# Optimization experiments

Measured on AMD Instinct MI355X. Metric: run time of the kernel, lower is better.

Reference implementation:

```python
import jax, jax.numpy as jnp
import numpy as np

CUTOFF = 1.5  # matches init cutoff
BIG = 1e6    # stand-in for masked-out (diagonal) distances


def _energy(positions, cell, sigma_matrix, epsilon_matrix, alpha_matrix, species):
    n = positions.shape[0]
    # pairwise displacements dr[i, j] = pos[j] - pos[i], minimum image under PBC
    dr = positions[None, :, :] - positions[:, None, :]          # [N, N, 3]
    inv_cell = jnp.linalg.inv(cell)
    frac = dr @ inv_cell
    frac = frac - jnp.round(frac)                               # minimum image
    dr = frac @ cell
    r2 = jnp.sum(dr * dr, axis=-1)                              # [N, N]
    eye = jnp.eye(n, dtype=bool)
    r = jnp.sqrt(jnp.where(eye, 1.0, r2))                       # safe sqrt on diag
    r = jnp.where(eye, BIG, r)                                  # mask self-pairs
    # species-pair parameter gather: [N, N]
    si, sj = species[:, None], species[None, :]
    sig = sigma_matrix[si, sj]
    eps = epsilon_matrix[si, sj]
    alp = alpha_matrix[si, sj]
    within = (r < CUTOFF) & (~eye)
    # soft-sphere pair energy: eps/alpha * (1 - r/sigma)^alpha for r < sigma
    f = jnp.maximum(1.0 - r / sig, 0.0)
    e = (eps / alp) * jnp.power(f, alp)
    e = jnp.where(within, e, 0.0)
    return jnp.sum(e) / 2.0


def setup_inputs() -> dict:
    key = jax.random.key(0)
    k1, k2, k3, k4, k5 = jax.random.split(key, 5)
    N, S = 4096, 8
    density = 0.8
    L = float((N / density) ** (1.0 / 3.0))
    positions = jax.random.uniform(k1, (N, 3), dtype=jnp.float32) * L
    cell = (L * jnp.eye(3)).astype(jnp.float32)
    species = jax.random.randint(k2, (N,), 0, S)

    def sym(k, base, scale):
        a = jax.random.uniform(k, (S, S), dtype=jnp.float32)
        a = 0.5 * (a + a.T)
        return base + scale * a

    sigma_matrix = sym(k3, 0.9, 0.2)    # ~1.0
    epsilon_matrix = sym(k4, 0.9, 0.2)  # ~1.0
    alpha_matrix = sym(k5, 2.0, 0.5)    # ~2.0-2.5
    return {
        "positions": positions,
        "cell": cell,
        "sigma_matrix": sigma_matrix,
        "epsilon_matrix": epsilon_matrix,
        "alpha_matrix": alpha_matrix,
        "species": species,
    }


def reference(positions, cell, sigma_matrix, epsilon_matrix, alpha_matrix, species):
    energy, g = jax.value_and_grad(
        lambda p: _energy(p, cell, sigma_matrix, epsilon_matrix, alpha_matrix, species)
    )(positions)
    forces = -g
    return energy, forces
```

## Files before the change

### kernel.cpp

```cpp
#include <hip/hip_runtime.h>


#define TI 256
#define TJ 64
#define CUT2 2.25f

__device__ __forceinline__ float fast_pow(float f, float e) {
    return __builtin_amdgcn_exp2f(e * __builtin_amdgcn_logf(f));
}

__global__ __launch_bounds__(TI) void soft_sphere_kernel(
    const float* __restrict__ pos,
    const float* __restrict__ cell,
    const float* __restrict__ sigm,
    const float* __restrict__ epsm,
    const float* __restrict__ alpm,
    const int*   __restrict__ spec,
    float*  __restrict__ out,
    float4* __restrict__ ws,
    int n)
{
    __shared__ float4 sh_pos[TJ];
    __shared__ float4 sh_tab[64];
    __shared__ float  sh_e[TI / 64];

    const int tid = threadIdx.x;
    const int j0  = blockIdx.y * TJ;

    if (tid < 64) {
        float sg = sigm[tid], ep = epsm[tid], al = alpm[tid];
        float inv_sg = 1.0f / sg;
        sh_tab[tid] = make_float4(inv_sg, al - 1.0f, ep / al, ep * inv_sg);
        int j = j0 + tid;
        sh_pos[tid] = make_float4(pos[3 * j + 0], pos[3 * j + 1],
                                  pos[3 * j + 2], __int_as_float(spec[j]));
    }

    const float m00 = cell[0], m01 = cell[1], m02 = cell[2];
    const float m10 = cell[3], m11 = cell[4], m12 = cell[5];
    const float m20 = cell[6], m21 = cell[7], m22 = cell[8];
    const bool diag = (m01 == 0.0f) & (m02 == 0.0f) & (m10 == 0.0f) &
                      (m12 == 0.0f) & (m20 == 0.0f) & (m21 == 0.0f);

    const int   i   = blockIdx.x * TI + tid;
    const float px  = pos[3 * i + 0];
    const float py  = pos[3 * i + 1];
    const float pz  = pos[3 * i + 2];
    const int   si8 = spec[i] << 3;

    __syncthreads();

    float e_acc = 0.0f, fxa = 0.0f, fya = 0.0f, fza = 0.0f;

    if (diag) {
        const float iLx = 1.0f / m00, iLy = 1.0f / m11, iLz = 1.0f / m22;
#pragma unroll 4
        for (int t = 0; t < TJ; ++t) {
            float4 pj = sh_pos[t];
            float dx = pj.x - px;
            float dy = pj.y - py;
            float dz = pj.z - pz;
            dx = fmaf(-rintf(dx * iLx), m00, dx);
            dy = fmaf(-rintf(dy * iLy), m11, dy);
            dz = fmaf(-rintf(dz * iLz), m22, dz);
            float r2 = fmaf(dx, dx, fmaf(dy, dy, dz * dz));
            if (r2 < CUT2 && (j0 + t) != i) {
                float4 tab = sh_tab[si8 + __float_as_int(pj.w)];
                float rinv = rsqrtf(r2);
                float r    = r2 * rinv;
                float f    = fmaf(-r, tab.x, 1.0f);
                if (f > 0.0f) {
                    float p = fast_pow(f, tab.y);
                    e_acc = fmaf(tab.z * p, f, e_acc);
                    float c = tab.w * p * rinv;
                    fxa = fmaf(-c, dx, fxa);
                    fya = fmaf(-c, dy, fya);
                    fza = fmaf(-c, dz, fza);
                }
            }
        }
    } else {
        const float det = m00 * (m11 * m22 - m12 * m21)
                        - m01 * (m10 * m22 - m12 * m20)
                        + m02 * (m10 * m21 - m11 * m20);
        const float rdet = 1.0f / det;
        const float i00 = (m11 * m22 - m12 * m21) * rdet;
        const float i01 = (m02 * m21 - m01 * m22) * rdet;
        const float i02 = (m01 * m12 - m02 * m11) * rdet;
        const float i10 = (m12 * m20 - m10 * m22) * rdet;
        const float i11 = (m00 * m22 - m02 * m20) * rdet;
        const float i12 = (m02 * m10 - m00 * m12) * rdet;
        const float i20 = (m10 * m21 - m11 * m20) * rdet;
        const float i21 = (m01 * m20 - m00 * m21) * rdet;
        const float i22 = (m00 * m11 - m01 * m10) * rdet;
#pragma unroll 2
        for (int t = 0; t < TJ; ++t) {
            float4 pj = sh_pos[t];
            float dx = pj.x - px, dy = pj.y - py, dz = pj.z - pz;
            float fx = dx * i00 + dy * i10 + dz * i20;
            float fy = dx * i01 + dy * i11 + dz * i21;
            float fz = dx * i02 + dy * i12 + dz * i22;
            fx -= rintf(fx); fy -= rintf(fy); fz -= rintf(fz);
            float ddx = fx * m00 + fy * m10 + fz * m20;
            float ddy = fx * m01 + fy * m11 + fz * m21;
            float ddz = fx * m02 + fy * m12 + fz * m22;
            float r2 = fmaf(ddx, ddx, fmaf(ddy, ddy, ddz * ddz));
            if (r2 < CUT2 && (j0 + t) != i) {
                float4 tab = sh_tab[si8 + __float_as_int(pj.w)];
                float rinv = rsqrtf(r2);
                float r    = r2 * rinv;
                float f    = fmaf(-r, tab.x, 1.0f);
                if (f > 0.0f) {
                    float p = fast_pow(f, tab.y);
                    e_acc = fmaf(tab.z * p, f, e_acc);
                    float c = tab.w * p * rinv;
                    fxa = fmaf(-c, ddx, fxa);
                    fya = fmaf(-c, ddy, fya);
                    fza = fmaf(-c, ddz, fza);
                }
            }
        }
    }

    if (ws != nullptr) {
        ws[(size_t)blockIdx.y * n + i] = make_float4(fxa, fya, fza, 0.0f);
    } else {
        atomicAdd(&out[1 + 3 * i + 0], fxa);
        atomicAdd(&out[1 + 3 * i + 1], fya);
        atomicAdd(&out[1 + 3 * i + 2], fza);
    }

    for (int off = 32; off > 0; off >>= 1)
        e_acc += __shfl_down(e_acc, off, 64);
    if ((tid & 63) == 0) sh_e[tid >> 6] = e_acc;
    __syncthreads();
    if (tid == 0) {
        float tot = 0.0f;
        for (int w = 0; w < TI / 64; ++w) tot += sh_e[w];
        atomicAdd(&out[0], 0.5f * tot);
    }
}

__global__ __launch_bounds__(256) void reduce_forces(
    const float* __restrict__ ws,
    float* __restrict__ out,
    int n, int nchunks)
{
    const int idx = blockIdx.x * 256 + threadIdx.x;
    const int total = 4 * n;
    if (idx >= total) return;
    float s = 0.0f;
#pragma unroll 8
    for (int c = 0; c < nchunks; ++c)
        s += ws[(size_t)c * total + idx];
    const int i = idx >> 2, d = idx & 3;
    if (d < 3) out[1 + 3 * i + d] = s;
}

extern "C" void kernel_launch(void* const* d_in, const int* in_sizes, int n_in,
                              void* d_out, int out_size, void* d_ws, size_t ws_size,
                              hipStream_t stream) {
    const float* pos  = (const float*)d_in[0];
    const float* cell = (const float*)d_in[1];
    const float* sigm = (const float*)d_in[2];
    const float* epsm = (const float*)d_in[3];
    const float* alpm = (const float*)d_in[4];
    const int*   spec = (const int*)d_in[5];
    float* out = (float*)d_out;
    const int n = in_sizes[5];

    const int nchunks = (n + TJ - 1) / TJ;
    const size_t ws_needed = (size_t)nchunks * n * sizeof(float4);
    const bool use_ws = (d_ws != nullptr) && (ws_size >= ws_needed);

    if (use_ws) {
        (void)hipMemsetAsync(out, 0, sizeof(float), stream);
    } else {
        size_t logical = (size_t)(1 + 3 * n);
        if ((size_t)out_size < logical) logical = (size_t)out_size;
        (void)hipMemsetAsync(out, 0, logical * sizeof(float), stream);
    }

    dim3 grid(n / TI, nchunks);
    soft_sphere_kernel<<<grid, TI, 0, stream>>>(
        pos, cell, sigm, epsm, alpm, spec, out,
        use_ws ? (float4*)d_ws : nullptr, n);

    if (use_ws) {
        int total = 4 * n;
        int blocks = (total + 255) / 256;
        reduce_forces<<<blocks, 256, 0, stream>>>((const float*)d_ws, out,
                                                  n, nchunks);
    }
}
```

Before: 92.79 us.

## Halve j-tile, add occupancy hint, reduce energy via workspace instead of atomics

Shrinks the j-chunk per block from 64 to 32, which doubles the grid to 16x128 blocks, and adds a launch-bounds occupancy hint of 8. Per-block energy partials are now written to a workspace and summed by an extra block in the force reduction kernel. This removes the energy memset and the global atomics. The cost is that the force partial workspace doubles in size, so the reduction kernel reads twice as much memory over twice as many chunks.

Measured after the change: 82.60 us. 11.0% less time.

```diff
diff --git a/kernel.cpp b/kernel.cpp
--- a/kernel.cpp
+++ b/kernel.cpp
@@ -2,14 +2,14 @@
 
 
 #define TI 256
-#define TJ 64
+#define TJ 32
 #define CUT2 2.25f
 
 __device__ __forceinline__ float fast_pow(float f, float e) {
     return __builtin_amdgcn_exp2f(e * __builtin_amdgcn_logf(f));
 }
 
-__global__ __launch_bounds__(TI) void soft_sphere_kernel(
+__global__ __launch_bounds__(TI, 8) void soft_sphere_kernel(
     const float* __restrict__ pos,
     const float* __restrict__ cell,
     const float* __restrict__ sigm,
@@ -18,6 +18,7 @@
     const int*   __restrict__ spec,
     float*  __restrict__ out,
     float4* __restrict__ ws,
+    float*  __restrict__ ews,
     int n)
 {
     __shared__ float4 sh_pos[TJ];
@@ -31,9 +32,11 @@
         float sg = sigm[tid], ep = epsm[tid], al = alpm[tid];
         float inv_sg = 1.0f / sg;
         sh_tab[tid] = make_float4(inv_sg, al - 1.0f, ep / al, ep * inv_sg);
-        int j = j0 + tid;
-        sh_pos[tid] = make_float4(pos[3 * j + 0], pos[3 * j + 1],
-                                  pos[3 * j + 2], __int_as_float(spec[j]));
+        if (tid < TJ) {
+            int j = j0 + tid;
+            sh_pos[tid] = make_float4(pos[3 * j + 0], pos[3 * j + 1],
+                                      pos[3 * j + 2], __int_as_float(spec[j]));
+        }
     }
 
     const float m00 = cell[0], m01 = cell[1], m02 = cell[2];
@@ -54,7 +57,7 @@
 
     if (diag) {
         const float iLx = 1.0f / m00, iLy = 1.0f / m11, iLz = 1.0f / m22;
-#pragma unroll 4
+#pragma unroll 8
         for (int t = 0; t < TJ; ++t) {
             float4 pj = sh_pos[t];
             float dx = pj.x - px;
@@ -137,20 +140,39 @@
     if (tid == 0) {
         float tot = 0.0f;
         for (int w = 0; w < TI / 64; ++w) tot += sh_e[w];
-        atomicAdd(&out[0], 0.5f * tot);
+        float half = 0.5f * tot;
+        if (ws != nullptr)
+            ews[blockIdx.y * gridDim.x + blockIdx.x] = half;
+        else
+            atomicAdd(&out[0], half);
     }
 }
 
 __global__ __launch_bounds__(256) void reduce_forces(
     const float* __restrict__ ws,
+    const float* __restrict__ ews,
     float* __restrict__ out,
-    int n, int nchunks)
+    int n, int nchunks, int nblocks)
 {
-    const int idx = blockIdx.x * 256 + threadIdx.x;
+    __shared__ float sh_e[4];
+    const int tid = threadIdx.x;
+
+    if ((int)blockIdx.x == gridDim.x - 1) {
+        float s = 0.0f;
+        for (int k = tid; k < nblocks; k += 256) s += ews[k];
+        for (int off = 32; off > 0; off >>= 1)
+            s += __shfl_down(s, off, 64);
+        if ((tid & 63) == 0) sh_e[tid >> 6] = s;
+        __syncthreads();
+        if (tid == 0)
+            out[0] = sh_e[0] + sh_e[1] + sh_e[2] + sh_e[3];
+        return;
+    }
+
+    const int idx = blockIdx.x * 256 + tid;
     const int total = 4 * n;
-    if (idx >= total) return;
     float s = 0.0f;
-#pragma unroll 8
+#pragma unroll 16
     for (int c = 0; c < nchunks; ++c)
         s += ws[(size_t)c * total + idx];
     const int i = idx >> 2, d = idx & 3;
@@ -169,13 +191,16 @@
     float* out = (float*)d_out;
     const int n = in_sizes[5];
 
-    const int nchunks = (n + TJ - 1) / TJ;
-    const size_t ws_needed = (size_t)nchunks * n * sizeof(float4);
+    const int nchunks  = (n + TJ - 1) / TJ;
+    const int nblocks  = (n / TI) * nchunks;
+    const size_t fbytes = (size_t)nchunks * n * sizeof(float4);
+    const size_t ws_needed = fbytes + (size_t)nblocks * sizeof(float);
     const bool use_ws = (d_ws != nullptr) && (ws_size >= ws_needed);
 
-    if (use_ws) {
-        (void)hipMemsetAsync(out, 0, sizeof(float), stream);
-    } else {
+    float4* fpart = use_ws ? (float4*)d_ws : nullptr;
+    float*  epart = use_ws ? (float*)((char*)d_ws + fbytes) : nullptr;
+
+    if (!use_ws) {
         size_t logical = (size_t)(1 + 3 * n);
         if ((size_t)out_size < logical) logical = (size_t)out_size;
         (void)hipMemsetAsync(out, 0, logical * sizeof(float), stream);
@@ -183,13 +208,11 @@
 
     dim3 grid(n / TI, nchunks);
     soft_sphere_kernel<<<grid, TI, 0, stream>>>(
-        pos, cell, sigm, epsm, alpm, spec, out,
-        use_ws ? (float4*)d_ws : nullptr, n);
+        pos, cell, sigm, epsm, alpm, spec, out, fpart, epart, n);
 
     if (use_ws) {
-        int total = 4 * n;
-        int blocks = (total + 255) / 256;
-        reduce_forces<<<blocks, 256, 0, stream>>>((const float*)d_ws, out,
-                                                  n, nchunks);
-    }
-}
+        int fb = (4 * n + 255) / 256;
+        reduce_forces<<<fb + 1, 256, 0, stream>>>(
+            (const float*)d_ws, epart, out, n, nchunks, nblocks);
+    }
+}
```
